# Kernel tuning notes

Measured on AMD Instinct MI355X. Metric: run time of the kernel, lower is better.

The kernel has to match this reference:

```python
import jax, jax.numpy as jnp
from jax import lax
import numpy as np

B, H, W, C = 4, 128, 128, 128   # C == d_route == n_heads, patch_len == H
OFFSET_RANGE = 5.0              # offset_range_factor == kernel == 5
SCALE = C ** -0.5               # self.scale_factor = d_route**-0.5
CYCLE = 168


def grid_sample_bilinear(img, grid):
    """torch.nn.functional.grid_sample(mode='bilinear', padding_mode='zeros', align_corners=False).
    img: (B,C,H,W); grid: (B,H,W,2) with (x,y) in [-1,1]."""
    Bn, Cn, Hn, Wn = img.shape
    xg = (grid[..., 0] + 1.0) * (Wn / 2.0) - 0.5
    yg = (grid[..., 1] + 1.0) * (Hn / 2.0) - 0.5
    x0 = jnp.floor(xg)
    y0 = jnp.floor(yg)
    img_flat = img.reshape(Bn, Cn, Hn * Wn)
    out = jnp.zeros_like(img)
    for xi in (x0, x0 + 1.0):
        for yi in (y0, y0 + 1.0):
            wgt = (1.0 - jnp.abs(xg - xi)) * (1.0 - jnp.abs(yg - yi))
            valid = (xi >= 0) & (xi <= Wn - 1) & (yi >= 0) & (yi <= Hn - 1)
            ix = jnp.clip(xi, 0, Wn - 1).astype(jnp.int32)
            iy = jnp.clip(yi, 0, Hn - 1).astype(jnp.int32)
            idx = (iy * Wn + ix).reshape(Bn, 1, -1)                      # (B,1,H*W)
            vals = jnp.take_along_axis(img_flat, idx, axis=2).reshape(Bn, Cn, Hn, Wn)
            out = out + vals * (wgt * valid.astype(img.dtype))[:, None, :, :]
    return out


def setup_inputs():
    key = jax.random.key(0)
    ks = jax.random.split(key, 12)
    s = C ** -0.5
    inp = {
        "x": jax.random.normal(ks[0], (B, H, W, C), dtype=jnp.float32),
        "cycle_index": jax.random.randint(ks[1], (B, 128), 0, CYCLE),  # dead path in cycle_mode='None'
        "Wq": jax.random.normal(ks[2], (C, C), dtype=jnp.float32) * s,
        "bq": jnp.zeros((C,), dtype=jnp.float32),
        "Wk": jax.random.normal(ks[3], (C, C), dtype=jnp.float32) * s,
        "bk": jnp.zeros((C,), dtype=jnp.float32),
        "Wv": jax.random.normal(ks[4], (C, C), dtype=jnp.float32) * s,
        "bv": jnp.zeros((C,), dtype=jnp.float32),
        "Wo": jax.random.normal(ks[5], (C, C), dtype=jnp.float32) * s,
        "bo": jnp.zeros((C,), dtype=jnp.float32),
        "Wc1": jax.random.normal(ks[6], (C, C, 5, 5), dtype=jnp.float32) * (1.0 / np.sqrt(C * 25)),
        "bc1": jnp.zeros((C,), dtype=jnp.float32),
        "Wc2": jax.random.normal(ks[7], (2, C), dtype=jnp.float32) * s,   # 1x1 conv, no bias
        "rel_bias": jax.random.normal(ks[8], (1, C, H, 1), dtype=jnp.float32) * 0.02,
    }
    return inp


def reference(x, cycle_index, Wq, bq, Wk, bk, Wv, bv, Wo, bo, Wc1, bc1, Wc2, rel_bias):
    Bn, Hn, Wn, Cn = x.shape
    xc = jnp.transpose(x, (0, 3, 1, 2))                                  # (B,C,H,W)
    # proj_q (1x1 conv) on x (cycle_mode='None')
    q = jnp.einsum('oc,bchw->bohw', Wq, xc) + bq[None, :, None, None]
    # proj_offset: 5x5 conv (pad 2) -> 1x1 conv to 2 channels, tanh * offset_range_factor
    c1 = lax.conv_general_dilated(q, Wc1, (1, 1), ((2, 2), (2, 2)),
                                  dimension_numbers=('NCHW', 'OIHW', 'NCHW')) + bc1[None, :, None, None]
    offset = jnp.tanh(jnp.einsum('oc,bchw->bohw', Wc2, c1)) * OFFSET_RANGE  # (B,2,H,W)
    # create_grid_like + normalize_grid (faithful, incl. x-coord normalized by H and vice versa)
    gx, gy = jnp.meshgrid(jnp.arange(Wn, dtype=x.dtype), jnp.arange(Hn, dtype=x.dtype), indexing='xy')
    grid = jnp.stack([gx, gy], axis=0)                                   # (2,H,W)
    vgrid = grid[None] + offset                                          # (B,2,H,W)
    gh = 2.0 * vgrid[:, 0] / max(Hn - 1, 1) - 1.0
    gw = 2.0 * vgrid[:, 1] / max(Wn - 1, 1) - 1.0
    sgrid = jnp.stack([gh, gw], axis=-1)                                 # (B,H,W,2) = (x,y) for grid_sample
    x_sampled = grid_sample_bilinear(xc, sgrid)                          # (B,C,H,W); n_groups=1 -> rearrange is identity
    k = (jnp.einsum('oc,bchw->bohw', Wk, x_sampled) + bk[None, :, None, None]).reshape(Bn * Cn, Hn, Wn)
    v = (jnp.einsum('oc,bchw->bohw', Wv, x_sampled) + bv[None, :, None, None] + rel_bias).reshape(Bn * Cn, Hn, Wn)
    qr = q.reshape(Bn * Cn, Hn, Wn)
    scores = jnp.einsum('bid,bjd->bij', qr, k) * SCALE                   # (B*C,H,H)
    attn = jax.nn.softmax(scores, axis=-1)
    out = jnp.einsum('bij,bjd->bid', attn, v)                            # (B*C,H,W)
    out = out.reshape(Bn, Hn, Wn, Cn)                                    # faithful raw reshape (as in original)
    return out @ Wo.T + bo
```

## Files before the change

kernel.cpp:

```cpp
#include <hip/hip_runtime.h>
#include <math.h>

#define IMG 16384

typedef short short4v __attribute__((ext_vector_type(4)));
typedef short short8  __attribute__((ext_vector_type(8)));
typedef float floatx4 __attribute__((ext_vector_type(4)));

__device__ __forceinline__ float4 ld4(const float* p) {
    return *reinterpret_cast<const float4*>(p);
}
__device__ __forceinline__ short f2bf(float f) {
    union { float f; unsigned u; } v; v.f = f;
    unsigned r = v.u + 0x7fffu + ((v.u >> 16) & 1u);
    return (short)(r >> 16);
}
__device__ __forceinline__ float bf2f(short s) {
    union { unsigned u; float f; } v;
    v.u = ((unsigned)(unsigned short)s) << 16;
    return v.f;
}

__launch_bounds__(256)
__global__ void k_wprep(const float* __restrict__ Wc1, const float* __restrict__ Wc2,
                        const float* __restrict__ bc1, const float* __restrict__ Wq,
                        const float* __restrict__ bq, const float* __restrict__ Wk,
                        const float* __restrict__ Wv, const float* __restrict__ Wo,
                        float* __restrict__ W2, float* __restrict__ cst,
                        float* __restrict__ b_eff, short* __restrict__ wbf,
                        short* __restrict__ w2h, short* __restrict__ w2l) {
    const int t = threadIdx.x;
    if (blockIdx.x >= 50) {
        if (blockIdx.x == 50) {
            for (int i = t; i < 14 * 128; i += 256) {
                w2h[6400 + i] = 0;
                w2l[6400 + i] = 0;
            }
        }
        int i = (blockIdx.x - 50) * 256 + t;
        int base = i * 8;
        int sel = base >> 14, off = base & 16383;
        const float* s = (sel == 0) ? Wq : (sel == 1) ? Wk : (sel == 2) ? Wv : Wo;
        float4 a = ld4(s + off), b = ld4(s + off + 4);
        short8 o;
        o[0] = f2bf(a.x); o[1] = f2bf(a.y); o[2] = f2bf(a.z); o[3] = f2bf(a.w);
        o[4] = f2bf(b.x); o[5] = f2bf(b.y); o[6] = f2bf(b.z); o[7] = f2bf(b.w);
        *reinterpret_cast<short8*>(wbf + base) = o;
        return;
    }
    __shared__ float U[128];
    __shared__ float red[256];
    __shared__ float wc2[128];
    __shared__ float bql[128];
    const int tt = blockIdx.x;
    const int tch = tt / 25, tap = tt % 25;
    if (t < 128) { wc2[t] = Wc2[tch * 128 + t]; bql[t] = bq[t]; }
    __syncthreads();
    const int c = t & 127, half = t >> 7;
    float p = 0.f;
    for (int o = half * 64; o < half * 64 + 64; ++o)
        p += wc2[o] * Wc1[(o * 128 + c) * 25 + tap];
    red[half * 128 + c] = p;
    __syncthreads();
    if (t < 128) U[t] = red[t] + red[128 + t];
    __syncthreads();
    float p2 = 0.f;
    for (int cc = half * 64; cc < half * 64 + 64; ++cc)
        p2 += U[cc] * Wq[cc * 128 + c];
    red[half * 128 + c] = p2;
    __syncthreads();
    if (t < 128) {
        float vv = red[t] + red[128 + t];
        W2[tt * 128 + t] = vv;
        short hh = f2bf(vv);
        w2h[tt * 128 + t] = hh;
        w2l[tt * 128 + t] = f2bf(vv - bf2f(hh));
    }
    if (t < 128) red[t] = U[t] * bql[t];
    __syncthreads();
    if (t == 0) {
        float s = 0.f;
        for (int j = 0; j < 128; ++j) s += red[j];
        cst[tt] = s;
    }
    if (tap == 0) {
        __syncthreads();
        if (t < 128) red[t] = wc2[t] * bc1[t];
        __syncthreads();
        if (t == 0) {
            float s = 0.f;
            for (int j = 0; j < 128; ++j) s += red[j];
            b_eff[tch] = s;
        }
    }
}

__launch_bounds__(256, 2)
__global__ void k_off(const float* __restrict__ x, const short* __restrict__ w2h,
                      const short* __restrict__ w2l, const float* __restrict__ cst,
                      float* __restrict__ P, short* __restrict__ x_bf) {
    __shared__ __align__(16) float stage[64 * 132];
    const int t = threadIdx.x;
    const int w = t >> 6, l = t & 63, l15 = l & 15, quad = l >> 4;
    const int p0 = blockIdx.x * 128;
    const int b = p0 >> 14, pix0 = p0 & (IMG - 1);

    floatx4 acc[2][4];
#pragma unroll
    for (int im = 0; im < 2; ++im)
#pragma unroll
        for (int in = 0; in < 4; ++in) acc[im][in] = (floatx4){0.f, 0.f, 0.f, 0.f};

    const float* xb = x + (size_t)p0 * 128;
    short* xbb = x_bf + (size_t)p0 * 128;

#pragma unroll
    for (int kc = 0; kc < 128; kc += 32) {
        short8 ah[2], al[2];
#pragma unroll
        for (int im = 0; im < 2; ++im) {
            int row = w * 32 + im * 16 + l15;
            const float* src = xb + row * 128 + kc + quad * 8;
            float4 f0 = ld4(src), f1 = ld4(src + 4);
            float fv[8] = {f0.x, f0.y, f0.z, f0.w, f1.x, f1.y, f1.z, f1.w};
            short8 h8, l8;
#pragma unroll
            for (int r = 0; r < 8; ++r) {
                short hh = f2bf(fv[r]);
                h8[r] = hh;
                l8[r] = f2bf(fv[r] - bf2f(hh));
            }
            ah[im] = h8; al[im] = l8;
            *reinterpret_cast<short8*>(xbb + row * 128 + kc + quad * 8) = h8;
        }
        short8 bh[4], bl[4];
#pragma unroll
        for (int in = 0; in < 4; ++in) {
            int o = in * 16 + l15;
            bh[in] = *reinterpret_cast<const short8*>(w2h + o * 128 + kc + quad * 8);
            bl[in] = *reinterpret_cast<const short8*>(w2l + o * 128 + kc + quad * 8);
        }
#pragma unroll
        for (int im = 0; im < 2; ++im)
#pragma unroll
            for (int in = 0; in < 4; ++in) {
                acc[im][in] = __builtin_amdgcn_mfma_f32_16x16x32_bf16(
                    ah[im], bh[in], acc[im][in], 0, 0, 0);
                acc[im][in] = __builtin_amdgcn_mfma_f32_16x16x32_bf16(
                    ah[im], bl[in], acc[im][in], 0, 0, 0);
                acc[im][in] = __builtin_amdgcn_mfma_f32_16x16x32_bf16(
                    al[im], bh[in], acc[im][in], 0, 0, 0);
            }
    }
#pragma unroll
    for (int im = 0; im < 2; ++im)
#pragma unroll
        for (int in = 0; in < 4; ++in) {
            int o = in * 16 + l15;
            int row0 = w * 32 + im * 16 + quad * 4;
            *reinterpret_cast<float4*>(&stage[o * 132 + row0]) =
                make_float4(acc[im][in][0], acc[im][in][1],
                            acc[im][in][2], acc[im][in][3]);
        }
    __syncthreads();
    for (int id = t; id < 50 * 32; id += 256) {
        int o = id >> 5, px4 = (id & 31) * 4;
        float c = cst[o];
        float4 v = *reinterpret_cast<float4*>(&stage[o * 132 + px4]);
        v.x += c; v.y += c; v.z += c; v.w += c;
        *reinterpret_cast<float4*>(P + ((size_t)(b * 50 + o)) * IMG + pix0 + px4) = v;
    }
}

__launch_bounds__(256, 2)
__global__ void k_fused3(const float* __restrict__ P, const float* __restrict__ b_eff,
                         const short* __restrict__ x_bf, const short* __restrict__ wbf,
                         const float* __restrict__ bq, const float* __restrict__ bk,
                         const float* __restrict__ bv, const float* __restrict__ rel,
                         short* __restrict__ q_bf, short* __restrict__ k_bf,
                         short* __restrict__ v_bf) {
    __shared__ __align__(16) char smem[70656];
    float* rowsP  = (float*)smem;
    short* stg    = (short*)smem;
    short* xsT    = (short*)(smem + 34816);
    float* offs_l = (float*)(smem + 69632);

    const int t = threadIdx.x;
    const int w = t >> 6, l = t & 63, l15 = l & 15, quad = l >> 4;
    const int mh = w >> 1, nh = w & 1;
    const int bh = blockIdx.x;
    const int b = bh >> 7, h = bh & 127;

    for (int id = t; id < 1600; id += 256) {
        int o = id >> 5, q4 = (id & 31) * 4;
        int di = (o % 25) / 5;
        int r = h + di - 2;
        int rc = min(max(r, 0), 127);
        float4 v = ld4(P + ((size_t)(b * 50 + o)) * IMG + rc * 128 + q4);
        float m = (r >= 0 && r < 128) ? 1.f : 0.f;
        v.x *= m; v.y *= m; v.z *= m; v.w *= m;
        *reinterpret_cast<float4*>(&rowsP[o * 136 + 4 + q4]) = v;
    }
    for (int id = t; id < 400; id += 256) {
        int o = id >> 3, c = id & 7;
        rowsP[o * 136 + (c < 4 ? c : 128 + c)] = 0.f;
    }
    __syncthreads();
    {
        int wp = t & 127, tc = t >> 7;
        float acc = 0.f;
#pragma unroll
        for (int di = 0; di < 5; ++di)
#pragma unroll
            for (int dj = 0; dj < 5; ++dj)
                acc += rowsP[(tc * 25 + di * 5 + dj) * 136 + wp + dj + 2];
        offs_l[tc * 128 + wp] = tanhf(acc + b_eff[tc]) * 5.0f;
    }
    __syncthreads();

    {
        const short* xbase = x_bf + (size_t)b * IMG * 128;
#pragma unroll
        for (int it = 0; it < 8; ++it) {
            int id = t + it * 256;
            int px = id >> 4, c8 = id & 15;
            float ox = offs_l[px];
            float oy = offs_l[128 + px];
            float xg = ((float)px + ox) * (128.0f / 127.0f) - 0.5f;
            float yg = ((float)h  + oy) * (128.0f / 127.0f) - 0.5f;
            float x0f = floorf(xg), y0f = floorf(yg);
            float fx = xg - x0f, fy = yg - y0f;
            int x0 = (int)x0f, y0 = (int)y0f;
            float s[8];
#pragma unroll
            for (int r = 0; r < 8; ++r) s[r] = 0.f;
#pragma unroll
            for (int tap = 0; tap < 4; ++tap) {
                int xi = x0 + (tap & 1), yi = y0 + (tap >> 1);
                float wgt = ((tap & 1) ? fx : 1.f - fx) * ((tap >> 1) ? fy : 1.f - fy);
                wgt = (xi >= 0 && xi < 128 && yi >= 0 && yi < 128) ? wgt : 0.f;
                int xc = min(max(xi, 0), 127), yc = min(max(yi, 0), 127);
                short8 v = *reinterpret_cast<const short8*>(
                    xbase + ((size_t)(yc * 128 + xc)) * 128 + c8 * 8);
#pragma unroll
                for (int r = 0; r < 8; ++r) s[r] = fmaf(wgt, bf2f(v[r]), s[r]);
            }
            short8 o;
#pragma unroll
            for (int r = 0; r < 8; ++r) o[r] = f2bf(s[r]);
            *reinterpret_cast<short8*>(&xsT[px * 136 + c8 * 8]) = o;
        }
    }

    {
        const short* xr = x_bf + ((size_t)(b * 128 + h)) * 128 * 128;
        floatx4 acc[4][4];
#pragma unroll
        for (int im = 0; im < 4; ++im)
#pragma unroll
            for (int in = 0; in < 4; ++in)
                acc[im][in] = (floatx4){0.f, 0.f, 0.f, 0.f};
#pragma unroll
        for (int kc = 0; kc < 128; kc += 32) {
            short8 af[4], bf_[4];
#pragma unroll
            for (int im = 0; im < 4; ++im)
                af[im] = *reinterpret_cast<const short8*>(
                    xr + (mh * 64 + im * 16 + l15) * 128 + kc + quad * 8);
#pragma unroll
            for (int in = 0; in < 4; ++in)
                bf_[in] = *reinterpret_cast<const short8*>(
                    wbf + (nh * 64 + in * 16 + l15) * 128 + kc + quad * 8);
#pragma unroll
            for (int im = 0; im < 4; ++im)
#pragma unroll
                for (int in = 0; in < 4; ++in)
                    acc[im][in] = __builtin_amdgcn_mfma_f32_16x16x32_bf16(
                        af[im], bf_[in], acc[im][in], 0, 0, 0);
        }
        __syncthreads();
#pragma unroll
        for (int in = 0; in < 4; ++in) {
            int o = nh * 64 + in * 16 + l15;
            float bb = bq[o];
#pragma unroll
            for (int im = 0; im < 4; ++im) {
                int row0 = mh * 64 + im * 16 + quad * 4;
                short4v s = {f2bf(acc[im][in][0] + bb), f2bf(acc[im][in][1] + bb),
                             f2bf(acc[im][in][2] + bb), f2bf(acc[im][in][3] + bb)};
                *reinterpret_cast<short4v*>(&stg[o * 136 + row0]) = s;
            }
        }
    }
    __syncthreads();
    for (int id = t; id < 2048; id += 256) {
        int o = id >> 4, seg = id & 15;
        *reinterpret_cast<short8*>(
            q_bf + ((size_t)(b * 128 + o)) * IMG + h * 128 + seg * 8)
            = *reinterpret_cast<const short8*>(&stg[o * 136 + seg * 8]);
    }

    {
        floatx4 ak[4][4], av[4][4];
#pragma unroll
        for (int im = 0; im < 4; ++im)
#pragma unroll
            for (int in = 0; in < 4; ++in) {
                ak[im][in] = (floatx4){0.f, 0.f, 0.f, 0.f};
                av[im][in] = (floatx4){0.f, 0.f, 0.f, 0.f};
            }
#pragma unroll
        for (int kc = 0; kc < 128; kc += 32) {
            short8 af[4], bk_[4], bv_[4];
#pragma unroll
            for (int im = 0; im < 4; ++im)
                af[im] = *reinterpret_cast<const short8*>(
                    &xsT[(mh * 64 + im * 16 + l15) * 136 + kc + quad * 8]);
#pragma unroll
            for (int in = 0; in < 4; ++in) {
                bk_[in] = *reinterpret_cast<const short8*>(
                    wbf + 16384 + (nh * 64 + in * 16 + l15) * 128 + kc + quad * 8);
                bv_[in] = *reinterpret_cast<const short8*>(
                    wbf + 32768 + (nh * 64 + in * 16 + l15) * 128 + kc + quad * 8);
            }
#pragma unroll
            for (int im = 0; im < 4; ++im)
#pragma unroll
                for (int in = 0; in < 4; ++in) {
                    ak[im][in] = __builtin_amdgcn_mfma_f32_16x16x32_bf16(
                        af[im], bk_[in], ak[im][in], 0, 0, 0);
                    av[im][in] = __builtin_amdgcn_mfma_f32_16x16x32_bf16(
                        af[im], bv_[in], av[im][in], 0, 0, 0);
                }
        }
        __syncthreads();
#pragma unroll
        for (int in = 0; in < 4; ++in) {
            int o = nh * 64 + in * 16 + l15;
            float bbk = bk[o];
            float bbv = bv[o] + rel[o * 128 + h];
#pragma unroll
            for (int im = 0; im < 4; ++im) {
                int row0 = mh * 64 + im * 16 + quad * 4;
                short4v sk = {f2bf(ak[im][in][0] + bbk), f2bf(ak[im][in][1] + bbk),
                              f2bf(ak[im][in][2] + bbk), f2bf(ak[im][in][3] + bbk)};
                short4v sv = {f2bf(av[im][in][0] + bbv), f2bf(av[im][in][1] + bbv),
                              f2bf(av[im][in][2] + bbv), f2bf(av[im][in][3] + bbv)};
                *reinterpret_cast<short4v*>(&stg[o * 136 + row0]) = sk;
                *reinterpret_cast<short4v*>(&xsT[o * 136 + row0]) = sv;
            }
        }
    }
    __syncthreads();
    for (int id = t; id < 4096; id += 256) {
        int sel = id >> 11;
        int o = (id >> 4) & 127, seg = id & 15;
        short* dst = sel ? v_bf : k_bf;
        const short* src = sel ? xsT : stg;
        *reinterpret_cast<short8*>(
            dst + ((size_t)(b * 128 + o)) * IMG + h * 128 + seg * 8)
            = *reinterpret_cast<const short8*>(&src[o * 136 + seg * 8]);
    }
}

__launch_bounds__(256, 2)
__global__ void k_attn3(const short* __restrict__ q_bf, const short* __restrict__ k_bf,
                        const short* __restrict__ v_bf, const short* __restrict__ WoB,
                        const float* __restrict__ bo, float* __restrict__ outp) {
    __shared__ __align__(16) short Pb[128 * 136];
    __shared__ __align__(16) short vT[128 * 136];
    __shared__ float redm[2 * 128];
    __shared__ float reds[2 * 128];

    const int t = threadIdx.x;
    const int w = t >> 6, l = t & 63, l15 = l & 15, quad = l >> 4;
    const int mh = w >> 1, nh = w & 1;
    const size_t hb = (size_t)blockIdx.x * IMG;
    const short* qp = q_bf + hb;
    const short* kp = k_bf + hb;
    const short* vp = v_bf + hb;

    for (int id = t; id < 2048; id += 256) {
        int j = id >> 4, seg = id & 15;
        short8 v8 = *reinterpret_cast<const short8*>(vp + j * 128 + seg * 8);
        int cbase = ((j >> 3) ^ seg) & 15;
        int off = j & 7;
#pragma unroll
        for (int r = 0; r < 8; ++r)
            vT[(seg * 8 + r) * 136 + cbase * 8 + off] = v8[r];
    }

    floatx4 acc[4][4];
#pragma unroll
    for (int im = 0; im < 4; ++im)
#pragma unroll
        for (int in = 0; in < 4; ++in)
            acc[im][in] = (floatx4){0.f, 0.f, 0.f, 0.f};

#pragma unroll
    for (int kc = 0; kc < 128; kc += 32) {
        short8 af[4], bf_[4];
#pragma unroll
        for (int im = 0; im < 4; ++im)
            af[im] = *reinterpret_cast<const short8*>(
                qp + (mh * 64 + im * 16 + l15) * 128 + kc + quad * 8);
#pragma unroll
        for (int in = 0; in < 4; ++in)
            bf_[in] = *reinterpret_cast<const short8*>(
                kp + (nh * 64 + in * 16 + l15) * 128 + kc + quad * 8);
#pragma unroll
        for (int im = 0; im < 4; ++im)
#pragma unroll
            for (int in = 0; in < 4; ++in)
                acc[im][in] = __builtin_amdgcn_mfma_f32_16x16x32_bf16(
                    af[im], bf_[in], acc[im][in], 0, 0, 0);
    }

    const float scale = 0.08838834764831845f;
    float mloc[4][4];
#pragma unroll
    for (int im = 0; im < 4; ++im)
#pragma unroll
        for (int r = 0; r < 4; ++r) {
            float m = acc[im][0][r];
#pragma unroll
            for (int in = 1; in < 4; ++in) m = fmaxf(m, acc[im][in][r]);
            mloc[im][r] = m;
        }
#pragma unroll
    for (int mask = 1; mask < 16; mask <<= 1)
#pragma unroll
        for (int im = 0; im < 4; ++im)
#pragma unroll
            for (int r = 0; r < 4; ++r)
                mloc[im][r] = fmaxf(mloc[im][r], __shfl_xor(mloc[im][r], mask, 64));
    if (l15 == 0) {
#pragma unroll
        for (int im = 0; im < 4; ++im)
#pragma unroll
            for (int r = 0; r < 4; ++r)
                redm[nh * 128 + mh * 64 + im * 16 + quad * 4 + r] = mloc[im][r];
    }
    __syncthreads();
    float sloc[4][4];
#pragma unroll
    for (int im = 0; im < 4; ++im)
#pragma unroll
        for (int r = 0; r < 4; ++r) {
            int row = mh * 64 + im * 16 + quad * 4 + r;
            float m = fmaxf(redm[row], redm[128 + row]);
            float ss = 0.f;
#pragma unroll
            for (int in = 0; in < 4; ++in) {
                float e = __expf((acc[im][in][r] - m) * scale);
                acc[im][in][r] = e;
                ss += e;
            }
            sloc[im][r] = ss;
        }
#pragma unroll
    for (int mask = 1; mask < 16; mask <<= 1)
#pragma unroll
        for (int im = 0; im < 4; ++im)
#pragma unroll
            for (int r = 0; r < 4; ++r)
                sloc[im][r] += __shfl_xor(sloc[im][r], mask, 64);
    if (l15 == 0) {
#pragma unroll
        for (int im = 0; im < 4; ++im)
#pragma unroll
            for (int r = 0; r < 4; ++r)
                reds[nh * 128 + mh * 64 + im * 16 + quad * 4 + r] = sloc[im][r];
    }
    __syncthreads();
#pragma unroll
    for (int im = 0; im < 4; ++im)
#pragma unroll
        for (int r = 0; r < 4; ++r) {
            int row = mh * 64 + im * 16 + quad * 4 + r;
            float inv = 1.0f / (reds[row] + reds[128 + row]);
#pragma unroll
            for (int in = 0; in < 4; ++in) {
                int col = nh * 64 + in * 16 + l15;
                Pb[row * 136 + col] = f2bf(acc[im][in][r] * inv);
            }
        }
    __syncthreads();

#pragma unroll
    for (int im = 0; im < 4; ++im)
#pragma unroll
        for (int in = 0; in < 4; ++in)
            acc[im][in] = (floatx4){0.f, 0.f, 0.f, 0.f};
#pragma unroll
    for (int kc = 0; kc < 128; kc += 32) {
        short8 af[4], bf_[4];
#pragma unroll
        for (int im = 0; im < 4; ++im)
            af[im] = *reinterpret_cast<const short8*>(
                &Pb[(mh * 64 + im * 16 + l15) * 136 + kc + quad * 8]);
#pragma unroll
        for (int in = 0; in < 4; ++in) {
            int dRow = nh * 64 + in * 16 + l15;
            int cphys = (((kc >> 3) + quad) ^ (dRow >> 3)) & 15;
            bf_[in] = *reinterpret_cast<const short8*>(
                &vT[dRow * 136 + cphys * 8]);
        }
#pragma unroll
        for (int im = 0; im < 4; ++im)
#pragma unroll
            for (int in = 0; in < 4; ++in)
                acc[im][in] = __builtin_amdgcn_mfma_f32_16x16x32_bf16(
                    af[im], bf_[in], acc[im][in], 0, 0, 0);
    }
    __syncthreads();
#pragma unroll
    for (int im = 0; im < 4; ++im)
#pragma unroll
        for (int in = 0; in < 4; ++in) {
            int col = nh * 64 + in * 16 + l15;
#pragma unroll
            for (int r = 0; r < 4; ++r) {
                int row = mh * 64 + im * 16 + quad * 4 + r;
                Pb[row * 136 + col] = f2bf(acc[im][in][r]);
            }
        }
    __syncthreads();

    float bb[4];
#pragma unroll
    for (int in = 0; in < 4; ++in) bb[in] = bo[nh * 64 + in * 16 + l15];
#pragma unroll
    for (int im = 0; im < 4; ++im)
#pragma unroll
        for (int in = 0; in < 4; ++in)
            acc[im][in] = (floatx4){0.f, 0.f, 0.f, 0.f};
#pragma unroll
    for (int kc = 0; kc < 128; kc += 32) {
        short8 af[4], bf_[4];
#pragma unroll
        for (int im = 0; im < 4; ++im)
            af[im] = *reinterpret_cast<const short8*>(
                &Pb[(mh * 64 + im * 16 + l15) * 136 + kc + quad * 8]);
#pragma unroll
        for (int in = 0; in < 4; ++in)
            bf_[in] = *reinterpret_cast<const short8*>(
                WoB + (nh * 64 + in * 16 + l15) * 128 + kc + quad * 8);
#pragma unroll
        for (int im = 0; im < 4; ++im)
#pragma unroll
            for (int in = 0; in < 4; ++in)
                acc[im][in] = __builtin_amdgcn_mfma_f32_16x16x32_bf16(
                    af[im], bf_[in], acc[im][in], 0, 0, 0);
    }
#pragma unroll
    for (int im = 0; im < 4; ++im)
#pragma unroll
        for (int in = 0; in < 4; ++in) {
            int col = nh * 64 + in * 16 + l15;
#pragma unroll
            for (int r = 0; r < 4; ++r) {
                int row = mh * 64 + im * 16 + quad * 4 + r;
                outp[hb + (size_t)row * 128 + col] = acc[im][in][r] + bb[in];
            }
        }
}

extern "C" void kernel_launch(void* const* d_in, const int* in_sizes, int n_in,
                              void* d_out, int out_size, void* d_ws, size_t ws_size,
                              hipStream_t stream) {
    const float* x   = (const float*)d_in[0];
    const float* Wq  = (const float*)d_in[2];
    const float* bq  = (const float*)d_in[3];
    const float* Wk  = (const float*)d_in[4];
    const float* bk  = (const float*)d_in[5];
    const float* Wv  = (const float*)d_in[6];
    const float* bv  = (const float*)d_in[7];
    const float* Wo  = (const float*)d_in[8];
    const float* bo  = (const float*)d_in[9];
    const float* Wc1 = (const float*)d_in[10];
    const float* bc1 = (const float*)d_in[11];
    const float* Wc2 = (const float*)d_in[12];
    const float* rel = (const float*)d_in[13];

    char* wsb = (char*)d_ws;
    short* q_bf  = (short*)(wsb);
    short* k_bf  = (short*)(wsb + 1ull * 16777216);
    short* v_bf  = (short*)(wsb + 2ull * 16777216);
    short* x_bf  = (short*)(wsb + 3ull * 16777216);
    float* P     = (float*)(wsb + 4ull * 16777216);
    float* W2    = (float*)(wsb + 4ull * 16777216 + 13107200);
    float* cst   = W2 + 6400;
    float* b_eff = cst + 64;
    short* wbf   = (short*)(b_eff + 16);
    short* w2h   = wbf + 65536;
    short* w2l   = w2h + 8192;
    float* outp  = (float*)d_out;

    hipLaunchKernelGGL(k_wprep,  dim3(82),   dim3(256), 0, stream, Wc1, Wc2, bc1, Wq, bq,
                       Wk, Wv, Wo, W2, cst, b_eff, wbf, w2h, w2l);
    hipLaunchKernelGGL(k_off,    dim3(512),  dim3(256), 0, stream, x, w2h, w2l, cst, P, x_bf);
    hipLaunchKernelGGL(k_fused3, dim3(512),  dim3(256), 0, stream, P, b_eff, x_bf, wbf,
                       bq, bk, bv, rel, q_bf, k_bf, v_bf);
    hipLaunchKernelGGL(k_attn3,  dim3(512),  dim3(256), 0, stream, q_bf, k_bf, v_bf,
                       wbf + 49152, bo, outp);
}
```

Before: 198.2 us.

## Split fused3 and attention kernels into half-row blocks to double grid size

Both k_fused3 and k_attn3 now launch 1024 blocks, each covering 64 pixels or query rows instead of 128. Shared memory per block shrinks and the launch-bound occupancy hints are raised (4 and 3 blocks per CU), which spreads the work across more of the MI355X CUs and leaves more waves resident to hide latency. The cost is redundant work per half: both halves of k_attn3 load all of K and V, and both halves of k_fused3 re-read the P halo and weights. The V transpose in attention now loads four rows at a time and writes short4 vectors into LDS.

New measurement: 219.7 us. +10.9%, slower.

```diff
diff --git a/kernel.cpp b/kernel.cpp
--- a/kernel.cpp
+++ b/kernel.cpp
@@ -172,62 +172,63 @@
     }
 }
 
-__launch_bounds__(256, 2)
+__launch_bounds__(256, 4)
 __global__ void k_fused3(const float* __restrict__ P, const float* __restrict__ b_eff,
                          const short* __restrict__ x_bf, const short* __restrict__ wbf,
                          const float* __restrict__ bq, const float* __restrict__ bk,
                          const float* __restrict__ bv, const float* __restrict__ rel,
                          short* __restrict__ q_bf, short* __restrict__ k_bf,
                          short* __restrict__ v_bf) {
-    __shared__ __align__(16) char smem[70656];
+    __shared__ __align__(16) char smem[37376];
     float* rowsP  = (float*)smem;
     short* stg    = (short*)smem;
-    short* xsT    = (short*)(smem + 34816);
-    float* offs_l = (float*)(smem + 69632);
+    short* xsT    = (short*)(smem + 18432);
+    short* vstg   = (short*)(smem + 18432);
+    float* offs_l = (float*)(smem + 36864);
 
     const int t = threadIdx.x;
     const int w = t >> 6, l = t & 63, l15 = l & 15, quad = l >> 4;
     const int mh = w >> 1, nh = w & 1;
-    const int bh = blockIdx.x;
-    const int b = bh >> 7, h = bh & 127;
-
-    for (int id = t; id < 1600; id += 256) {
-        int o = id >> 5, q4 = (id & 31) * 4;
+    const int b = blockIdx.x >> 8, h = (blockIdx.x >> 1) & 127;
+    const int half = blockIdx.x & 1;
+    const int px0 = half << 6;
+    const int c0 = px0 - 4;
+
+    for (int id = t; id < 900; id += 256) {
+        int o = id / 18, c4 = id % 18;
         int di = (o % 25) / 5;
         int r = h + di - 2;
+        int gc = c0 + c4 * 4;
         int rc = min(max(r, 0), 127);
-        float4 v = ld4(P + ((size_t)(b * 50 + o)) * IMG + rc * 128 + q4);
-        float m = (r >= 0 && r < 128) ? 1.f : 0.f;
+        int gcc = min(max(gc, 0), 124);
+        float4 v = ld4(P + ((size_t)(b * 50 + o)) * IMG + rc * 128 + gcc);
+        float m = (r >= 0 && r < 128 && gc >= 0 && gc <= 124) ? 1.f : 0.f;
         v.x *= m; v.y *= m; v.z *= m; v.w *= m;
-        *reinterpret_cast<float4*>(&rowsP[o * 136 + 4 + q4]) = v;
-    }
-    for (int id = t; id < 400; id += 256) {
-        int o = id >> 3, c = id & 7;
-        rowsP[o * 136 + (c < 4 ? c : 128 + c)] = 0.f;
-    }
-    __syncthreads();
-    {
-        int wp = t & 127, tc = t >> 7;
+        *reinterpret_cast<float4*>(&rowsP[o * 72 + c4 * 4]) = v;
+    }
+    __syncthreads();
+    if (t < 128) {
+        int tc = t >> 6, wp = t & 63;
         float acc = 0.f;
 #pragma unroll
         for (int di = 0; di < 5; ++di)
 #pragma unroll
             for (int dj = 0; dj < 5; ++dj)
-                acc += rowsP[(tc * 25 + di * 5 + dj) * 136 + wp + dj + 2];
-        offs_l[tc * 128 + wp] = tanhf(acc + b_eff[tc]) * 5.0f;
+                acc += rowsP[(tc * 25 + di * 5 + dj) * 72 + wp + dj + 2];
+        offs_l[tc * 64 + wp] = tanhf(acc + b_eff[tc]) * 5.0f;
     }
     __syncthreads();
 
     {
         const short* xbase = x_bf + (size_t)b * IMG * 128;
 #pragma unroll
-        for (int it = 0; it < 8; ++it) {
+        for (int it = 0; it < 4; ++it) {
             int id = t + it * 256;
-            int px = id >> 4, c8 = id & 15;
-            float ox = offs_l[px];
-            float oy = offs_l[128 + px];
-            float xg = ((float)px + ox) * (128.0f / 127.0f) - 0.5f;
-            float yg = ((float)h  + oy) * (128.0f / 127.0f) - 0.5f;
+            int pl = id >> 4, c8 = id & 15;
+            float ox = offs_l[pl];
+            float oy = offs_l[64 + pl];
+            float xg = ((float)(px0 + pl) + ox) * (128.0f / 127.0f) - 0.5f;
+            float yg = ((float)h + oy) * (128.0f / 127.0f) - 0.5f;
             float x0f = floorf(xg), y0f = floorf(yg);
             float fx = xg - x0f, fy = yg - y0f;
             int x0 = (int)x0f, y0 = (int)y0f;
@@ -248,31 +249,31 @@
             short8 o;
 #pragma unroll
             for (int r = 0; r < 8; ++r) o[r] = f2bf(s[r]);
-            *reinterpret_cast<short8*>(&xsT[px * 136 + c8 * 8]) = o;
+            *reinterpret_cast<short8*>(&xsT[pl * 136 + c8 * 8]) = o;
         }
     }
 
     {
         const short* xr = x_bf + ((size_t)(b * 128 + h)) * 128 * 128;
-        floatx4 acc[4][4];
-#pragma unroll
-        for (int im = 0; im < 4; ++im)
+        floatx4 acc[2][4];
+#pragma unroll
+        for (int im = 0; im < 2; ++im)
 #pragma unroll
             for (int in = 0; in < 4; ++in)
                 acc[im][in] = (floatx4){0.f, 0.f, 0.f, 0.f};
 #pragma unroll
         for (int kc = 0; kc < 128; kc += 32) {
-            short8 af[4], bf_[4];
-#pragma unroll
-            for (int im = 0; im < 4; ++im)
+            short8 af[2], bf_[4];
+#pragma unroll
+            for (int im = 0; im < 2; ++im)
                 af[im] = *reinterpret_cast<const short8*>(
-                    xr + (mh * 64 + im * 16 + l15) * 128 + kc + quad * 8);
+                    xr + (px0 + mh * 32 + im * 16 + l15) * 128 + kc + quad * 8);
 #pragma unroll
             for (int in = 0; in < 4; ++in)
                 bf_[in] = *reinterpret_cast<const short8*>(
                     wbf + (nh * 64 + in * 16 + l15) * 128 + kc + quad * 8);
 #pragma unroll
-            for (int im = 0; im < 4; ++im)
+            for (int im = 0; im < 2; ++im)
 #pragma unroll
                 for (int in = 0; in < 4; ++in)
                     acc[im][in] = __builtin_amdgcn_mfma_f32_16x16x32_bf16(
@@ -284,26 +285,26 @@
             int o = nh * 64 + in * 16 + l15;
             float bb = bq[o];
 #pragma unroll
-            for (int im = 0; im < 4; ++im) {
-                int row0 = mh * 64 + im * 16 + quad * 4;
+            for (int im = 0; im < 2; ++im) {
+                int row0 = mh * 32 + im * 16 + quad * 4;
                 short4v s = {f2bf(acc[im][in][0] + bb), f2bf(acc[im][in][1] + bb),
                              f2bf(acc[im][in][2] + bb), f2bf(acc[im][in][3] + bb)};
-                *reinterpret_cast<short4v*>(&stg[o * 136 + row0]) = s;
-            }
-        }
-    }
-    __syncthreads();
-    for (int id = t; id < 2048; id += 256) {
-        int o = id >> 4, seg = id & 15;
+                *reinterpret_cast<short4v*>(&stg[o * 72 + row0]) = s;
+            }
+        }
+    }
+    __syncthreads();
+    for (int id = t; id < 1024; id += 256) {
+        int o = id >> 3, seg = id & 7;
         *reinterpret_cast<short8*>(
-            q_bf + ((size_t)(b * 128 + o)) * IMG + h * 128 + seg * 8)
-            = *reinterpret_cast<const short8*>(&stg[o * 136 + seg * 8]);
+            q_bf + ((size_t)(b * 128 + o)) * IMG + h * 128 + px0 + seg * 8)
+            = *reinterpret_cast<const short8*>(&stg[o * 72 + seg * 8]);
     }
 
     {
-        floatx4 ak[4][4], av[4][4];
-#pragma unroll
-        for (int im = 0; im < 4; ++im)
+        floatx4 ak[2][4], av[2][4];
+#pragma unroll
+        for (int im = 0; im < 2; ++im)
 #pragma unroll
             for (int in = 0; in < 4; ++in) {
                 ak[im][in] = (floatx4){0.f, 0.f, 0.f, 0.f};
@@ -311,11 +312,11 @@
             }
 #pragma unroll
         for (int kc = 0; kc < 128; kc += 32) {
-            short8 af[4], bk_[4], bv_[4];
-#pragma unroll
-            for (int im = 0; im < 4; ++im)
+            short8 af[2], bk_[4], bv_[4];
+#pragma unroll
+            for (int im = 0; im < 2; ++im)
                 af[im] = *reinterpret_cast<const short8*>(
-                    &xsT[(mh * 64 + im * 16 + l15) * 136 + kc + quad * 8]);
+                    &xsT[(mh * 32 + im * 16 + l15) * 136 + kc + quad * 8]);
 #pragma unroll
             for (int in = 0; in < 4; ++in) {
                 bk_[in] = *reinterpret_cast<const short8*>(
@@ -324,7 +325,7 @@
                     wbf + 32768 + (nh * 64 + in * 16 + l15) * 128 + kc + quad * 8);
             }
 #pragma unroll
-            for (int im = 0; im < 4; ++im)
+            for (int im = 0; im < 2; ++im)
 #pragma unroll
                 for (int in = 0; in < 4; ++in) {
                     ak[im][in] = __builtin_amdgcn_mfma_f32_16x16x32_bf16(
@@ -340,76 +341,82 @@
             float bbk = bk[o];
             float bbv = bv[o] + rel[o * 128 + h];
 #pragma unroll
-            for (int im = 0; im < 4; ++im) {
-                int row0 = mh * 64 + im * 16 + quad * 4;
+            for (int im = 0; im < 2; ++im) {
+                int row0 = mh * 32 + im * 16 + quad * 4;
                 short4v sk = {f2bf(ak[im][in][0] + bbk), f2bf(ak[im][in][1] + bbk),
                               f2bf(ak[im][in][2] + bbk), f2bf(ak[im][in][3] + bbk)};
                 short4v sv = {f2bf(av[im][in][0] + bbv), f2bf(av[im][in][1] + bbv),
                               f2bf(av[im][in][2] + bbv), f2bf(av[im][in][3] + bbv)};
-                *reinterpret_cast<short4v*>(&stg[o * 136 + row0]) = sk;
-                *reinterpret_cast<short4v*>(&xsT[o * 136 + row0]) = sv;
-            }
-        }
-    }
-    __syncthreads();
-    for (int id = t; id < 4096; id += 256) {
-        int sel = id >> 11;
-        int o = (id >> 4) & 127, seg = id & 15;
+                *reinterpret_cast<short4v*>(&stg[o * 72 + row0]) = sk;
+                *reinterpret_cast<short4v*>(&vstg[o * 72 + row0]) = sv;
+            }
+        }
+    }
+    __syncthreads();
+    for (int id = t; id < 2048; id += 256) {
+        int sel = id >> 10;
+        int o = (id >> 3) & 127, seg = id & 7;
         short* dst = sel ? v_bf : k_bf;
-        const short* src = sel ? xsT : stg;
+        const short* src = sel ? vstg : stg;
         *reinterpret_cast<short8*>(
-            dst + ((size_t)(b * 128 + o)) * IMG + h * 128 + seg * 8)
-            = *reinterpret_cast<const short8*>(&src[o * 136 + seg * 8]);
-    }
-}
-
-__launch_bounds__(256, 2)
+            dst + ((size_t)(b * 128 + o)) * IMG + h * 128 + px0 + seg * 8)
+            = *reinterpret_cast<const short8*>(&src[o * 72 + seg * 8]);
+    }
+}
+
+__launch_bounds__(256, 3)
 __global__ void k_attn3(const short* __restrict__ q_bf, const short* __restrict__ k_bf,
                         const short* __restrict__ v_bf, const short* __restrict__ WoB,
                         const float* __restrict__ bo, float* __restrict__ outp) {
-    __shared__ __align__(16) short Pb[128 * 136];
     __shared__ __align__(16) short vT[128 * 136];
-    __shared__ float redm[2 * 128];
-    __shared__ float reds[2 * 128];
+    __shared__ __align__(16) short Pb[64 * 136];
+    __shared__ float redm[2 * 64];
+    __shared__ float reds[2 * 64];
 
     const int t = threadIdx.x;
     const int w = t >> 6, l = t & 63, l15 = l & 15, quad = l >> 4;
     const int mh = w >> 1, nh = w & 1;
-    const size_t hb = (size_t)blockIdx.x * IMG;
+    const size_t hb = (size_t)(blockIdx.x >> 1) * IMG;
+    const int i0 = (blockIdx.x & 1) << 6;
     const short* qp = q_bf + hb;
     const short* kp = k_bf + hb;
     const short* vp = v_bf + hb;
 
-    for (int id = t; id < 2048; id += 256) {
-        int j = id >> 4, seg = id & 15;
-        short8 v8 = *reinterpret_cast<const short8*>(vp + j * 128 + seg * 8);
-        int cbase = ((j >> 3) ^ seg) & 15;
-        int off = j & 7;
-#pragma unroll
-        for (int r = 0; r < 8; ++r)
-            vT[(seg * 8 + r) * 136 + cbase * 8 + off] = v8[r];
-    }
-
-    floatx4 acc[4][4];
-#pragma unroll
-    for (int im = 0; im < 4; ++im)
+    for (int id = t; id < 512; id += 256) {
+        int j4 = id >> 4, seg = id & 15;
+        const short* src = vp + (j4 * 4) * 128 + seg * 8;
+        short8 v0 = *reinterpret_cast<const short8*>(src);
+        short8 v1 = *reinterpret_cast<const short8*>(src + 128);
+        short8 v2 = *reinterpret_cast<const short8*>(src + 256);
+        short8 v3 = *reinterpret_cast<const short8*>(src + 384);
+        int phys = (((j4 >> 1) ^ seg) & 15) * 8 + (j4 & 1) * 4;
+#pragma unroll
+        for (int r = 0; r < 8; ++r) {
+            short4v wv = {v0[r], v1[r], v2[r], v3[r]};
+            *reinterpret_cast<short4v*>(&vT[(seg * 8 + r) * 136 + phys]) = wv;
+        }
+    }
+
+    floatx4 acc[2][4];
+#pragma unroll
+    for (int im = 0; im < 2; ++im)
 #pragma unroll
         for (int in = 0; in < 4; ++in)
             acc[im][in] = (floatx4){0.f, 0.f, 0.f, 0.f};
 
 #pragma unroll
     for (int kc = 0; kc < 128; kc += 32) {
-        short8 af[4], bf_[4];
-#pragma unroll
-        for (int im = 0; im < 4; ++im)
+        short8 af[2], bf_[4];
+#pragma unroll
+        for (int im = 0; im < 2; ++im)
             af[im] = *reinterpret_cast<const short8*>(
-                qp + (mh * 64 + im * 16 + l15) * 128 + kc + quad * 8);
+                qp + (i0 + mh * 32 + im * 16 + l15) * 128 + kc + quad * 8);
 #pragma unroll
         for (int in = 0; in < 4; ++in)
             bf_[in] = *reinterpret_cast<const short8*>(
                 kp + (nh * 64 + in * 16 + l15) * 128 + kc + quad * 8);
 #pragma unroll
-        for (int im = 0; im < 4; ++im)
+        for (int im = 0; im < 2; ++im)
 #pragma unroll
             for (int in = 0; in < 4; ++in)
                 acc[im][in] = __builtin_amdgcn_mfma_f32_16x16x32_bf16(
@@ -417,9 +424,9 @@
     }
 
     const float scale = 0.08838834764831845f;
-    float mloc[4][4];
-#pragma unroll
-    for (int im = 0; im < 4; ++im)
+    float mloc[2][4];
+#pragma unroll
+    for (int im = 0; im < 2; ++im)
 #pragma unroll
         for (int r = 0; r < 4; ++r) {
             float m = acc[im][0][r];
@@ -430,25 +437,25 @@
 #pragma unroll
     for (int mask = 1; mask < 16; mask <<= 1)
 #pragma unroll
-        for (int im = 0; im < 4; ++im)
+        for (int im = 0; im < 2; ++im)
 #pragma unroll
             for (int r = 0; r < 4; ++r)
                 mloc[im][r] = fmaxf(mloc[im][r], __shfl_xor(mloc[im][r], mask, 64));
     if (l15 == 0) {
 #pragma unroll
-        for (int im = 0; im < 4; ++im)
+        for (int im = 0; im < 2; ++im)
 #pragma unroll
             for (int r = 0; r < 4; ++r)
-                redm[nh * 128 + mh * 64 + im * 16 + quad * 4 + r] = mloc[im][r];
-    }
-    __syncthreads();
-    float sloc[4][4];
-#pragma unroll
-    for (int im = 0; im < 4; ++im)
+                redm[nh * 64 + mh * 32 + im * 16 + quad * 4 + r] = mloc[im][r];
+    }
+    __syncthreads();
+    float sloc[2][4];
+#pragma unroll
+    for (int im = 0; im < 2; ++im)
 #pragma unroll
         for (int r = 0; r < 4; ++r) {
-            int row = mh * 64 + im * 16 + quad * 4 + r;
-            float m = fmaxf(redm[row], redm[128 + row]);
+            int row = mh * 32 + im * 16 + quad * 4 + r;
+            float m = fmaxf(redm[row], redm[64 + row]);
             float ss = 0.f;
 #pragma unroll
             for (int in = 0; in < 4; ++in) {
@@ -461,24 +468,24 @@
 #pragma unroll
     for (int mask = 1; mask < 16; mask <<= 1)
 #pragma unroll
-        for (int im = 0; im < 4; ++im)
+        for (int im = 0; im < 2; ++im)
 #pragma unroll
             for (int r = 0; r < 4; ++r)
                 sloc[im][r] += __shfl_xor(sloc[im][r], mask, 64);
     if (l15 == 0) {
 #pragma unroll
-        for (int im = 0; im < 4; ++im)
+        for (int im = 0; im < 2; ++im)
 #pragma unroll
             for (int r = 0; r < 4; ++r)
-                reds[nh * 128 + mh * 64 + im * 16 + quad * 4 + r] = sloc[im][r];
-    }
-    __syncthreads();
-#pragma unroll
-    for (int im = 0; im < 4; ++im)
+                reds[nh * 64 + mh * 32 + im * 16 + quad * 4 + r] = sloc[im][r];
+    }
+    __syncthreads();
+#pragma unroll
+    for (int im = 0; im < 2; ++im)
 #pragma unroll
         for (int r = 0; r < 4; ++r) {
-            int row = mh * 64 + im * 16 + quad * 4 + r;
-            float inv = 1.0f / (reds[row] + reds[128 + row]);
+            int row = mh * 32 + im * 16 + quad * 4 + r;
+            float inv = 1.0f / (reds[row] + reds[64 + row]);
 #pragma unroll
             for (int in = 0; in < 4; ++in) {
                 int col = nh * 64 + in * 16 + l15;
@@ -488,17 +495,17 @@
     __syncthreads();
 
 #pragma unroll
-    for (int im = 0; im < 4; ++im)
+    for (int im = 0; im < 2; ++im)
 #pragma unroll
         for (int in = 0; in < 4; ++in)
             acc[im][in] = (floatx4){0.f, 0.f, 0.f, 0.f};
 #pragma unroll
     for (int kc = 0; kc < 128; kc += 32) {
-        short8 af[4], bf_[4];
-#pragma unroll
-        for (int im = 0; im < 4; ++im)
+        short8 af[2], bf_[4];
+#pragma unroll
+        for (int im = 0; im < 2; ++im)
             af[im] = *reinterpret_cast<const short8*>(
-                &Pb[(mh * 64 + im * 16 + l15) * 136 + kc + quad * 8]);
+                &Pb[(mh * 32 + im * 16 + l15) * 136 + kc + quad * 8]);
 #pragma unroll
         for (int in = 0; in < 4; ++in) {
             int dRow = nh * 64 + in * 16 + l15;
@@ -507,7 +514,7 @@
                 &vT[dRow * 136 + cphys * 8]);
         }
 #pragma unroll
-        for (int im = 0; im < 4; ++im)
+        for (int im = 0; im < 2; ++im)
 #pragma unroll
             for (int in = 0; in < 4; ++in)
                 acc[im][in] = __builtin_amdgcn_mfma_f32_16x16x32_bf16(
@@ -515,13 +522,13 @@
     }
     __syncthreads();
 #pragma unroll
-    for (int im = 0; im < 4; ++im)
+    for (int im = 0; im < 2; ++im)
 #pragma unroll
         for (int in = 0; in < 4; ++in) {
             int col = nh * 64 + in * 16 + l15;
 #pragma unroll
             for (int r = 0; r < 4; ++r) {
-                int row = mh * 64 + im * 16 + quad * 4 + r;
+                int row = mh * 32 + im * 16 + quad * 4 + r;
                 Pb[row * 136 + col] = f2bf(acc[im][in][r]);
             }
         }
@@ -531,37 +538,37 @@
 #pragma unroll
     for (int in = 0; in < 4; ++in) bb[in] = bo[nh * 64 + in * 16 + l15];
 #pragma unroll
-    for (int im = 0; im < 4; ++im)
+    for (int im = 0; im < 2; ++im)
 #pragma unroll
         for (int in = 0; in < 4; ++in)
             acc[im][in] = (floatx4){0.f, 0.f, 0.f, 0.f};
 #pragma unroll
     for (int kc = 0; kc < 128; kc += 32) {
-        short8 af[4], bf_[4];
-#pragma unroll
-        for (int im = 0; im < 4; ++im)
+        short8 af[2], bf_[4];
+#pragma unroll
+        for (int im = 0; im < 2; ++im)
             af[im] = *reinterpret_cast<const short8*>(
-                &Pb[(mh * 64 + im * 16 + l15) * 136 + kc + quad * 8]);
+                &Pb[(mh * 32 + im * 16 + l15) * 136 + kc + quad * 8]);
 #pragma unroll
         for (int in = 0; in < 4; ++in)
             bf_[in] = *reinterpret_cast<const short8*>(
                 WoB + (nh * 64 + in * 16 + l15) * 128 + kc + quad * 8);
 #pragma unroll
-        for (int im = 0; im < 4; ++im)
+        for (int im = 0; im < 2; ++im)
 #pragma unroll
             for (int in = 0; in < 4; ++in)
                 acc[im][in] = __builtin_amdgcn_mfma_f32_16x16x32_bf16(
                     af[im], bf_[in], acc[im][in], 0, 0, 0);
     }
 #pragma unroll
-    for (int im = 0; im < 4; ++im)
+    for (int im = 0; im < 2; ++im)
 #pragma unroll
         for (int in = 0; in < 4; ++in) {
             int col = nh * 64 + in * 16 + l15;
 #pragma unroll
             for (int r = 0; r < 4; ++r) {
-                int row = mh * 64 + im * 16 + quad * 4 + r;
-                outp[hb + (size_t)row * 128 + col] = acc[im][in][r] + bb[in];
+                int row = mh * 32 + im * 16 + quad * 4 + r;
+                outp[hb + (size_t)(i0 + row) * 128 + col] = acc[im][in][r] + bb[in];
             }
         }
 }
@@ -600,8 +607,8 @@
     hipLaunchKernelGGL(k_wprep,  dim3(82),   dim3(256), 0, stream, Wc1, Wc2, bc1, Wq, bq,
                        Wk, Wv, Wo, W2, cst, b_eff, wbf, w2h, w2l);
     hipLaunchKernelGGL(k_off,    dim3(512),  dim3(256), 0, stream, x, w2h, w2l, cst, P, x_bf);
-    hipLaunchKernelGGL(k_fused3, dim3(512),  dim3(256), 0, stream, P, b_eff, x_bf, wbf,
+    hipLaunchKernelGGL(k_fused3, dim3(1024), dim3(256), 0, stream, P, b_eff, x_bf, wbf,
                        bq, bk, bv, rel, q_bf, k_bf, v_bf);
-    hipLaunchKernelGGL(k_attn3,  dim3(512),  dim3(256), 0, stream, q_bf, k_bf, v_bf,
+    hipLaunchKernelGGL(k_attn3,  dim3(1024), dim3(256), 0, stream, q_bf, k_bf, v_bf,
                        wbf + 49152, bo, outp);
 }
```
